# Kernel tuning notes

Measured on AMD Instinct MI355X. Metric: run time of the kernel, lower is better.

Reference implementation:

```python
import jax, jax.numpy as jnp
import numpy as np

HIDDEN = 512
NUM_HEADS = 8


def setup_inputs() -> dict:
    key = jax.random.key(0)
    ks = jax.random.split(key, 8)
    Tq, Tk, Cq, Ck, H = 1, 65536, 512, 512, HIDDEN
    s = 1.0 / np.sqrt(H)
    return {
        "Q": jax.random.normal(ks[0], (Tq, Cq), jnp.float32),
        "K": jax.random.normal(ks[1], (Tk, Ck), jnp.float32),
        "Wq": jax.random.normal(ks[2], (H, Cq), jnp.float32) * s,
        "bq": jax.random.normal(ks[3], (H,), jnp.float32) * s,
        "Wk": jax.random.normal(ks[4], (H, Ck), jnp.float32) * s,
        "bk": jax.random.normal(ks[5], (H,), jnp.float32) * s,
        "Wout": jax.random.normal(ks[6], (1, NUM_HEADS), jnp.float32) * 0.3,
        "bout": jax.random.normal(ks[7], (1,), jnp.float32) * 0.3,
    }


def reference(Q, K, Wq, bq, Wk, bk, Wout, bout):
    h = NUM_HEADS
    H = Wq.shape[0]
    d = H // h  # per-head dim
    # linear + ReLU projections
    Ql = jax.nn.relu(Q @ Wq.T + bq)          # [1, H]
    Kl = jax.nn.relu(K @ Wk.T + bk)          # [Tk, H]
    # split into heads (T_q == 1 is required by linear_out)
    Qh = Ql.reshape(h, d)                    # [h, d]
    Kh = Kl.reshape(-1, h, d)                # [Tk, h, d]
    # per-head scores, scaled by sqrt(d_head); dropout rate 0 -> identity
    scores = jnp.einsum('hd,thd->th', Qh, Kh) / (d ** 0.5)  # [Tk, h]
    # learned per-head fusion, then softmax over the T_k axis
    logits = scores @ Wout.T + bout          # [Tk, 1]
    return jax.nn.softmax(logits, axis=0)    # [Tk, 1]
```

## Files before the change

kernel.cpp:

```cpp
#include <hip/hip_runtime.h>
#include <hip/hip_fp16.h>

#define CDIM 512
#define ROWS 65536
#define BM   256

typedef _Float16 half8  __attribute__((ext_vector_type(8)));
typedef __fp16   fp16x2 __attribute__((ext_vector_type(2)));
typedef float    f32x16 __attribute__((ext_vector_type(16)));

#define GLD_LDS16(gp, lp) __builtin_amdgcn_global_load_lds( \
    (const __attribute__((address_space(1))) unsigned int*)(gp), \
    (__attribute__((address_space(3))) unsigned int*)(lp), 16, 0, 0)

__device__ __forceinline__ half8 cvt8(float4 f0, float4 f1) {
    union { fp16x2 h2[4]; half8 h8; } u;
    u.h2[0] = __builtin_amdgcn_cvt_pkrtz(f0.x, f0.y);
    u.h2[1] = __builtin_amdgcn_cvt_pkrtz(f0.z, f0.w);
    u.h2[2] = __builtin_amdgcn_cvt_pkrtz(f1.x, f1.y);
    u.h2[3] = __builtin_amdgcn_cvt_pkrtz(f1.z, f1.w);
    return u.h8;
}

__global__ void prep_kernel(const float* __restrict__ Q, const float* __restrict__ Wq,
                            const float* __restrict__ bq, const float* __restrict__ Wout,
                            const float* __restrict__ Wk,
                            float* __restrict__ v, _Float16* __restrict__ Wkf) {
    __shared__ float qs[CDIM];
    const int t = threadIdx.x;
    if (blockIdx.x < 32) {
        qs[t] = Q[t]; qs[t + 256] = Q[t + 256];
        __syncthreads();
        const int jj  = t >> 4;
        const int sub = t & 15;
        const int j   = blockIdx.x * 16 + jj;
        const float4* w4 = (const float4*)(Wq + (size_t)j * CDIM + sub * 32);
        const float4* q4 = (const float4*)(qs + sub * 32);
        float s = 0.f;
        #pragma unroll
        for (int i = 0; i < 8; ++i) {
            float4 w = w4[i]; float4 q = q4[i];
            s = fmaf(w.x, q.x, s); s = fmaf(w.y, q.y, s);
            s = fmaf(w.z, q.z, s); s = fmaf(w.w, q.w, s);
        }
        s += __shfl_xor(s, 1); s += __shfl_xor(s, 2);
        s += __shfl_xor(s, 4); s += __shfl_xor(s, 8);
        if (sub == 0) {
            s += bq[j];
            s = fmaxf(s, 0.f);
            v[j] = s * Wout[j >> 6] * 0.125f;
        }
    } else {
        const int gid = (blockIdx.x - 32) * 256 + t;
        const int jb  = gid >> 11;
        const int kc  = (gid >> 6) & 31;
        const int l   = gid & 63;
        const int j   = jb * 32 + (l & 31);
        const int k   = kc * 16 + (l >> 5) * 8;
        const float* src = Wk + (size_t)j * CDIM + k;
        float4 f0 = *(const float4*)(src);
        float4 f1 = *(const float4*)(src + 4);
        *(half8*)(Wkf + (size_t)gid * 8) = cvt8(f0, f1);
    }
}

__global__ __launch_bounds__(512, 1) void score_kernel(
    const float* __restrict__ Kmat, const _Float16* __restrict__ Wkf,
    const float* __restrict__ bk, const float* __restrict__ v,
    float* __restrict__ partial2)
{
    __shared__ alignas(16) char Ab[2][32768];
    __shared__ alignas(16) char Bbuf[2][32768];
    __shared__ float scr[2][4][128];

    const int tid  = threadIdx.x;
    const int lane = tid & 63;
    const int wave = tid >> 6;
    const int l31  = lane & 31;
    const int lhi  = lane >> 5;
    const int wm   = wave >> 2;
    const int wn   = wave & 3;
    const int cls  = blockIdx.y;
    const int rowbase = blockIdx.x * BM;

    const float* gA = Kmat + (size_t)(rowbase + wave * 32 + l31) * CDIM + lhi * 8;
    const _Float16* gB = Wkf + ((size_t)(cls * 8 + wave) * 32) * 512;

    f32x16 acc[4][2];
    #pragma unroll
    for (int mb = 0; mb < 4; ++mb)
        #pragma unroll
        for (int b = 0; b < 2; ++b)
            #pragma unroll
            for (int r = 0; r < 16; ++r) acc[mb][b][r] = 0.f;

    #pragma unroll
    for (int kc = 0; kc < 4; ++kc) {
        float4 f0 = *(const float4*)(gA + kc * 16);
        float4 f1 = *(const float4*)(gA + kc * 16 + 4);
        *(half8*)(Ab[0] + (wave * 4 + kc) * 1024 + lane * 16) = cvt8(f0, f1);
        GLD_LDS16(gB + (size_t)kc * 512 + lane * 8, Bbuf[0] + (wave * 4 + kc) * 1024);
    }
    float4 R[4][2];
    #pragma unroll
    for (int kc = 0; kc < 4; ++kc) {
        R[kc][0] = *(const float4*)(gA + 64 + kc * 16);
        R[kc][1] = *(const float4*)(gA + 64 + kc * 16 + 4);
    }
    __syncthreads();

    #pragma unroll
    for (int ks = 0; ks < 8; ++ks) {
        const int cur = ks & 1;
        if (ks < 7) {
            #pragma unroll
            for (int kc = 0; kc < 4; ++kc) {
                *(half8*)(Ab[cur ^ 1] + (wave * 4 + kc) * 1024 + lane * 16)
                    = cvt8(R[kc][0], R[kc][1]);
                GLD_LDS16(gB + (size_t)((ks + 1) * 4 + kc) * 512 + lane * 8,
                          Bbuf[cur ^ 1] + (wave * 4 + kc) * 1024);
            }
        }
        if (ks < 6) {
            #pragma unroll
            for (int kc = 0; kc < 4; ++kc) {
                R[kc][0] = *(const float4*)(gA + (ks + 2) * 64 + kc * 16);
                R[kc][1] = *(const float4*)(gA + (ks + 2) * 64 + kc * 16 + 4);
            }
        }
        __builtin_amdgcn_sched_barrier(0);
        #pragma unroll
        for (int kc = 0; kc < 4; ++kc) {
            half8 a0 = *(const half8*)(Ab[cur] + ((wm * 4 + 0) * 4 + kc) * 1024 + lane * 16);
            half8 a1 = *(const half8*)(Ab[cur] + ((wm * 4 + 1) * 4 + kc) * 1024 + lane * 16);
            half8 a2 = *(const half8*)(Ab[cur] + ((wm * 4 + 2) * 4 + kc) * 1024 + lane * 16);
            half8 a3 = *(const half8*)(Ab[cur] + ((wm * 4 + 3) * 4 + kc) * 1024 + lane * 16);
            half8 b0 = *(const half8*)(Bbuf[cur] + ((wn * 2 + 0) * 4 + kc) * 1024 + lane * 16);
            half8 b1 = *(const half8*)(Bbuf[cur] + ((wn * 2 + 1) * 4 + kc) * 1024 + lane * 16);
            acc[0][0] = __builtin_amdgcn_mfma_f32_32x32x16_f16(a0, b0, acc[0][0], 0, 0, 0);
            acc[1][0] = __builtin_amdgcn_mfma_f32_32x32x16_f16(a1, b0, acc[1][0], 0, 0, 0);
            acc[2][0] = __builtin_amdgcn_mfma_f32_32x32x16_f16(a2, b0, acc[2][0], 0, 0, 0);
            acc[3][0] = __builtin_amdgcn_mfma_f32_32x32x16_f16(a3, b0, acc[3][0], 0, 0, 0);
            acc[0][1] = __builtin_amdgcn_mfma_f32_32x32x16_f16(a0, b1, acc[0][1], 0, 0, 0);
            acc[1][1] = __builtin_amdgcn_mfma_f32_32x32x16_f16(a1, b1, acc[1][1], 0, 0, 0);
            acc[2][1] = __builtin_amdgcn_mfma_f32_32x32x16_f16(a2, b1, acc[2][1], 0, 0, 0);
            acc[3][1] = __builtin_amdgcn_mfma_f32_32x32x16_f16(a3, b1, acc[3][1], 0, 0, 0);
        }
        __syncthreads();
    }

    const int j0 = (cls * 8 + wn * 2 + 0) * 32 + l31;
    const int j1 = (cls * 8 + wn * 2 + 1) * 32 + l31;
    const float bj0 = bk[j0], vj0 = v[j0];
    const float bj1 = bk[j1], vj1 = v[j1];

    #pragma unroll
    for (int mb = 0; mb < 4; ++mb) {
        float part[16];
        #pragma unroll
        for (int r = 0; r < 16; ++r)
            part[r] = fmaxf(acc[mb][0][r] + bj0, 0.f) * vj0
                    + fmaxf(acc[mb][1][r] + bj1, 0.f) * vj1;

        float q0[8];
        #pragma unroll
        for (int i = 0; i < 8; ++i) {
            const bool b = lane & 1;
            float keep = b ? part[i + 8] : part[i];
            float send = b ? part[i] : part[i + 8];
            q0[i] = keep + __shfl_xor(send, 1);
        }
        float q1[4];
        #pragma unroll
        for (int i = 0; i < 4; ++i) {
            const bool b = lane & 2;
            float keep = b ? q0[i + 4] : q0[i];
            float send = b ? q0[i] : q0[i + 4];
            q1[i] = keep + __shfl_xor(send, 2);
        }
        float q2[2];
        #pragma unroll
        for (int i = 0; i < 2; ++i) {
            const bool b = lane & 4;
            float keep = b ? q1[i + 2] : q1[i];
            float send = b ? q1[i] : q1[i + 2];
            q2[i] = keep + __shfl_xor(send, 4);
        }
        float q3;
        {
            const bool b = lane & 8;
            float keep = b ? q2[1] : q2[0];
            float send = b ? q2[0] : q2[1];
            q3 = keep + __shfl_xor(send, 8);
        }
        float s = q3 + __shfl_xor(q3, 16);
        if (l31 < 16) {
            const int rr  = ((l31 & 1) << 3) | ((l31 & 2) << 1) | ((l31 & 4) >> 1) | ((l31 & 8) >> 3);
            const int row = (rr & 3) + 8 * (rr >> 2) + 4 * lhi;
            scr[wm][wn][mb * 32 + row] = s;
        }
    }
    __syncthreads();

    if (tid < 256) {
        const int wmx = tid >> 7;
        const int idx = tid & 127;
        float s = scr[wmx][0][idx] + scr[wmx][1][idx] + scr[wmx][2][idx] + scr[wmx][3][idx];
        partial2[(size_t)cls * ROWS + rowbase + wmx * 128 + idx] = s;
    }
}

__global__ void expsum_kernel(const float* __restrict__ partial2, float* __restrict__ logits,
                              float* __restrict__ blocksum) {
    __shared__ float red[256];
    const int t = threadIdx.x;
    const int row = blockIdx.x * 256 + t;
    const float lg = partial2[row] + partial2[ROWS + row];
    logits[row] = lg;
    red[t] = expf(lg);
    __syncthreads();
    for (int s = 128; s > 0; s >>= 1) {
        if (t < s) red[t] += red[t + s];
        __syncthreads();
    }
    if (t == 0) blocksum[blockIdx.x] = red[0];
}

__global__ void norm_kernel(const float* __restrict__ logits, const float* __restrict__ blocksum,
                            float* __restrict__ out) {
    __shared__ float red[256];
    const int t = threadIdx.x;
    red[t] = blocksum[t];
    __syncthreads();
    for (int s = 128; s > 0; s >>= 1) {
        if (t < s) red[t] += red[t + s];
        __syncthreads();
    }
    const float zinv = 1.0f / red[0];
    const int i = blockIdx.x * 256 + t;
    out[i] = expf(logits[i]) * zinv;
}

extern "C" void kernel_launch(void* const* d_in, const int* in_sizes, int n_in,
                              void* d_out, int out_size, void* d_ws, size_t ws_size,
                              hipStream_t stream) {
    const float* Q    = (const float*)d_in[0];
    const float* Kmat = (const float*)d_in[1];
    const float* Wq   = (const float*)d_in[2];
    const float* bq   = (const float*)d_in[3];
    const float* Wk   = (const float*)d_in[4];
    const float* bk   = (const float*)d_in[5];
    const float* Wout = (const float*)d_in[6];
    float* out = (float*)d_out;

    char* ws = (char*)d_ws;
    _Float16* Wkf   = (_Float16*)(ws);
    float* v        = (float*)(ws + 524288);
    float* partial2 = (float*)(ws + 526336);
    float* logits   = (float*)(ws + 1050624);
    float* blocksum = (float*)(ws + 1312768);

    hipLaunchKernelGGL(prep_kernel,   dim3(160),     dim3(256), 0, stream, Q, Wq, bq, Wout, Wk, v, Wkf);
    hipLaunchKernelGGL(score_kernel,  dim3(256, 2),  dim3(512), 0, stream, Kmat, Wkf, bk, v, partial2);
    hipLaunchKernelGGL(expsum_kernel, dim3(256),     dim3(256), 0, stream, partial2, logits, blocksum);
    hipLaunchKernelGGL(norm_kernel,   dim3(256),     dim3(256), 0, stream, logits, blocksum, out);
}
```

Before: 71.58 us.

## Shrink score GEMM tile to 128x256 with 256-thread blocks, two per CU

Restructures the score GEMM to use 128-row by 256-column tiles, 4 waves per block and 2 blocks per CU, with a 32-wide K step over 16 iterations instead of 64-wide over 8. Each wave now computes 2x4 MFMA tiles instead of 4x2. The A-tile fp16 conversion moves to after the MFMA loop, so global loads overlap compute. This is meant to double the grid to 1024 blocks and raise occupancy and latency hiding. In exchange there are more barriers, a shorter K depth per step, and the Wk tile is reloaded by twice as many blocks.

Result: faster. 64.57 us (-9.8%).

```diff
diff --git a/kernel.cpp b/kernel.cpp
--- a/kernel.cpp
+++ b/kernel.cpp
@@ -3,7 +3,7 @@
 
 #define CDIM 512
 #define ROWS 65536
-#define BM   256
+#define NSTEPS 16
 
 typedef _Float16 half8  __attribute__((ext_vector_type(8)));
 typedef __fp16   fp16x2 __attribute__((ext_vector_type(2)));
@@ -64,103 +64,119 @@
     }
 }
 
-__global__ __launch_bounds__(512, 1) void score_kernel(
+__global__ __launch_bounds__(256, 2) void score_kernel(
     const float* __restrict__ Kmat, const _Float16* __restrict__ Wkf,
     const float* __restrict__ bk, const float* __restrict__ v,
     float* __restrict__ partial2)
 {
-    __shared__ alignas(16) char Ab[2][32768];
-    __shared__ alignas(16) char Bbuf[2][32768];
-    __shared__ float scr[2][4][128];
+    __shared__ alignas(16) char Ab[2][8192];
+    __shared__ alignas(16) char Bb[2][16384];
+    __shared__ float scr[4][2][32];
 
     const int tid  = threadIdx.x;
     const int lane = tid & 63;
     const int wave = tid >> 6;
     const int l31  = lane & 31;
     const int lhi  = lane >> 5;
-    const int wm   = wave >> 2;
-    const int wn   = wave & 3;
+    const int wm   = wave >> 1;
+    const int wn   = wave & 1;
     const int cls  = blockIdx.y;
-    const int rowbase = blockIdx.x * BM;
+    const int rowbase = blockIdx.x * 128;
 
     const float* gA = Kmat + (size_t)(rowbase + wave * 32 + l31) * CDIM + lhi * 8;
-    const _Float16* gB = Wkf + ((size_t)(cls * 8 + wave) * 32) * 512;
-
-    f32x16 acc[4][2];
-    #pragma unroll
-    for (int mb = 0; mb < 4; ++mb)
-        #pragma unroll
-        for (int b = 0; b < 2; ++b)
-            #pragma unroll
-            for (int r = 0; r < 16; ++r) acc[mb][b][r] = 0.f;
-
-    #pragma unroll
-    for (int kc = 0; kc < 4; ++kc) {
-        float4 f0 = *(const float4*)(gA + kc * 16);
-        float4 f1 = *(const float4*)(gA + kc * 16 + 4);
-        *(half8*)(Ab[0] + (wave * 4 + kc) * 1024 + lane * 16) = cvt8(f0, f1);
-        GLD_LDS16(gB + (size_t)kc * 512 + lane * 8, Bbuf[0] + (wave * 4 + kc) * 1024);
-    }
-    float4 R[4][2];
-    #pragma unroll
-    for (int kc = 0; kc < 4; ++kc) {
-        R[kc][0] = *(const float4*)(gA + 64 + kc * 16);
-        R[kc][1] = *(const float4*)(gA + 64 + kc * 16 + 4);
-    }
-    __syncthreads();
-
-    #pragma unroll
-    for (int ks = 0; ks < 8; ++ks) {
+    const char* gB = (const char*)Wkf + (size_t)(cls * 8) * 32768;
+
+    f32x16 acc[2][4];
+    #pragma unroll
+    for (int mb = 0; mb < 2; ++mb)
+        #pragma unroll
+        for (int nb = 0; nb < 4; ++nb)
+            #pragma unroll
+            for (int r = 0; r < 16; ++r) acc[mb][nb][r] = 0.f;
+
+    #pragma unroll
+    for (int kcl = 0; kcl < 2; ++kcl) {
+        float4 f0 = *(const float4*)(gA + kcl * 16);
+        float4 f1 = *(const float4*)(gA + kcl * 16 + 4);
+        *(half8*)(Ab[0] + (wave * 2 + kcl) * 1024 + lane * 16) = cvt8(f0, f1);
+        #pragma unroll
+        for (int nbl = 0; nbl < 2; ++nbl) {
+            const int nb = wave * 2 + nbl;
+            GLD_LDS16(gB + ((size_t)nb * 32 + kcl) * 1024 + lane * 16,
+                      Bb[0] + (nb * 2 + kcl) * 1024 + lane * 16);
+        }
+    }
+    __syncthreads();
+
+    float4 R[2][2];
+
+    for (int ks = 0; ks < NSTEPS; ++ks) {
         const int cur = ks & 1;
-        if (ks < 7) {
-            #pragma unroll
-            for (int kc = 0; kc < 4; ++kc) {
-                *(half8*)(Ab[cur ^ 1] + (wave * 4 + kc) * 1024 + lane * 16)
-                    = cvt8(R[kc][0], R[kc][1]);
-                GLD_LDS16(gB + (size_t)((ks + 1) * 4 + kc) * 512 + lane * 8,
-                          Bbuf[cur ^ 1] + (wave * 4 + kc) * 1024);
+        const bool pf = (ks + 1 < NSTEPS);
+
+        if (pf) {
+            const float* ga = gA + (ks + 1) * 32;
+            #pragma unroll
+            for (int kcl = 0; kcl < 2; ++kcl) {
+                R[kcl][0] = *(const float4*)(ga + kcl * 16);
+                R[kcl][1] = *(const float4*)(ga + kcl * 16 + 4);
+                #pragma unroll
+                for (int nbl = 0; nbl < 2; ++nbl) {
+                    const int nb = wave * 2 + nbl;
+                    GLD_LDS16(gB + ((size_t)nb * 32 + (ks + 1) * 2 + kcl) * 1024 + lane * 16,
+                              Bb[cur ^ 1] + (nb * 2 + kcl) * 1024 + lane * 16);
+                }
             }
         }
-        if (ks < 6) {
-            #pragma unroll
-            for (int kc = 0; kc < 4; ++kc) {
-                R[kc][0] = *(const float4*)(gA + (ks + 2) * 64 + kc * 16);
-                R[kc][1] = *(const float4*)(gA + (ks + 2) * 64 + kc * 16 + 4);
-            }
-        }
         __builtin_amdgcn_sched_barrier(0);
-        #pragma unroll
-        for (int kc = 0; kc < 4; ++kc) {
-            half8 a0 = *(const half8*)(Ab[cur] + ((wm * 4 + 0) * 4 + kc) * 1024 + lane * 16);
-            half8 a1 = *(const half8*)(Ab[cur] + ((wm * 4 + 1) * 4 + kc) * 1024 + lane * 16);
-            half8 a2 = *(const half8*)(Ab[cur] + ((wm * 4 + 2) * 4 + kc) * 1024 + lane * 16);
-            half8 a3 = *(const half8*)(Ab[cur] + ((wm * 4 + 3) * 4 + kc) * 1024 + lane * 16);
-            half8 b0 = *(const half8*)(Bbuf[cur] + ((wn * 2 + 0) * 4 + kc) * 1024 + lane * 16);
-            half8 b1 = *(const half8*)(Bbuf[cur] + ((wn * 2 + 1) * 4 + kc) * 1024 + lane * 16);
+
+        #pragma unroll
+        for (int kcl = 0; kcl < 2; ++kcl) {
+            half8 a0 = *(const half8*)(Ab[cur] + ((wm * 2 + 0) * 2 + kcl) * 1024 + lane * 16);
+            half8 a1 = *(const half8*)(Ab[cur] + ((wm * 2 + 1) * 2 + kcl) * 1024 + lane * 16);
+            half8 b0 = *(const half8*)(Bb[cur] + ((wn * 4 + 0) * 2 + kcl) * 1024 + lane * 16);
+            half8 b1 = *(const half8*)(Bb[cur] + ((wn * 4 + 1) * 2 + kcl) * 1024 + lane * 16);
+            half8 b2 = *(const half8*)(Bb[cur] + ((wn * 4 + 2) * 2 + kcl) * 1024 + lane * 16);
+            half8 b3 = *(const half8*)(Bb[cur] + ((wn * 4 + 3) * 2 + kcl) * 1024 + lane * 16);
             acc[0][0] = __builtin_amdgcn_mfma_f32_32x32x16_f16(a0, b0, acc[0][0], 0, 0, 0);
+            acc[0][1] = __builtin_amdgcn_mfma_f32_32x32x16_f16(a0, b1, acc[0][1], 0, 0, 0);
+            acc[0][2] = __builtin_amdgcn_mfma_f32_32x32x16_f16(a0, b2, acc[0][2], 0, 0, 0);
+            acc[0][3] = __builtin_amdgcn_mfma_f32_32x32x16_f16(a0, b3, acc[0][3], 0, 0, 0);
             acc[1][0] = __builtin_amdgcn_mfma_f32_32x32x16_f16(a1, b0, acc[1][0], 0, 0, 0);
-            acc[2][0] = __builtin_amdgcn_mfma_f32_32x32x16_f16(a2, b0, acc[2][0], 0, 0, 0);
-            acc[3][0] = __builtin_amdgcn_mfma_f32_32x32x16_f16(a3, b0, acc[3][0], 0, 0, 0);
-            acc[0][1] = __builtin_amdgcn_mfma_f32_32x32x16_f16(a0, b1, acc[0][1], 0, 0, 0);
             acc[1][1] = __builtin_amdgcn_mfma_f32_32x32x16_f16(a1, b1, acc[1][1], 0, 0, 0);
-            acc[2][1] = __builtin_amdgcn_mfma_f32_32x32x16_f16(a2, b1, acc[2][1], 0, 0, 0);
-            acc[3][1] = __builtin_amdgcn_mfma_f32_32x32x16_f16(a3, b1, acc[3][1], 0, 0, 0);
-        }
-        __syncthreads();
-    }
-
-    const int j0 = (cls * 8 + wn * 2 + 0) * 32 + l31;
-    const int j1 = (cls * 8 + wn * 2 + 1) * 32 + l31;
-    const float bj0 = bk[j0], vj0 = v[j0];
-    const float bj1 = bk[j1], vj1 = v[j1];
-
-    #pragma unroll
-    for (int mb = 0; mb < 4; ++mb) {
+            acc[1][2] = __builtin_amdgcn_mfma_f32_32x32x16_f16(a1, b2, acc[1][2], 0, 0, 0);
+            acc[1][3] = __builtin_amdgcn_mfma_f32_32x32x16_f16(a1, b3, acc[1][3], 0, 0, 0);
+        }
+        __builtin_amdgcn_sched_barrier(0);
+
+        if (pf) {
+            #pragma unroll
+            for (int kcl = 0; kcl < 2; ++kcl)
+                *(half8*)(Ab[cur ^ 1] + (wave * 2 + kcl) * 1024 + lane * 16)
+                    = cvt8(R[kcl][0], R[kcl][1]);
+        }
+        __syncthreads();
+    }
+
+    float bj[4], vj[4];
+    #pragma unroll
+    for (int nb = 0; nb < 4; ++nb) {
+        const int j = cls * 256 + (wn * 4 + nb) * 32 + l31;
+        bj[nb] = bk[j];
+        vj[nb] = v[j];
+    }
+
+    #pragma unroll
+    for (int mb = 0; mb < 2; ++mb) {
         float part[16];
         #pragma unroll
-        for (int r = 0; r < 16; ++r)
-            part[r] = fmaxf(acc[mb][0][r] + bj0, 0.f) * vj0
-                    + fmaxf(acc[mb][1][r] + bj1, 0.f) * vj1;
+        for (int r = 0; r < 16; ++r) {
+            float s = 0.f;
+            #pragma unroll
+            for (int nb = 0; nb < 4; ++nb)
+                s += fmaxf(acc[mb][nb][r] + bj[nb], 0.f) * vj[nb];
+            part[r] = s;
+        }
 
         float q0[8];
         #pragma unroll
@@ -197,16 +213,15 @@
         if (l31 < 16) {
             const int rr  = ((l31 & 1) << 3) | ((l31 & 2) << 1) | ((l31 & 4) >> 1) | ((l31 & 8) >> 3);
             const int row = (rr & 3) + 8 * (rr >> 2) + 4 * lhi;
-            scr[wm][wn][mb * 32 + row] = s;
-        }
-    }
-    __syncthreads();
-
-    if (tid < 256) {
-        const int wmx = tid >> 7;
-        const int idx = tid & 127;
-        float s = scr[wmx][0][idx] + scr[wmx][1][idx] + scr[wmx][2][idx] + scr[wmx][3][idx];
-        partial2[(size_t)cls * ROWS + rowbase + wmx * 128 + idx] = s;
+            scr[wm * 2 + mb][wn][row] = s;
+        }
+    }
+    __syncthreads();
+
+    if (tid < 128) {
+        const int rb = tid >> 5;
+        const int r  = tid & 31;
+        partial2[(size_t)cls * ROWS + rowbase + rb * 32 + r] = scr[rb][0][r] + scr[rb][1][r];
     }
 }
 
@@ -261,7 +276,7 @@
     float* blocksum = (float*)(ws + 1312768);
 
     hipLaunchKernelGGL(prep_kernel,   dim3(160),     dim3(256), 0, stream, Q, Wq, bq, Wout, Wk, v, Wkf);
-    hipLaunchKernelGGL(score_kernel,  dim3(256, 2),  dim3(512), 0, stream, Kmat, Wkf, bk, v, partial2);
+    hipLaunchKernelGGL(score_kernel,  dim3(512, 2),  dim3(256), 0, stream, Kmat, Wkf, bk, v, partial2);
     hipLaunchKernelGGL(expsum_kernel, dim3(256),     dim3(256), 0, stream, partial2, logits, blocksum);
     hipLaunchKernelGGL(norm_kernel,   dim3(256),     dim3(256), 0, stream, logits, blocksum, out);
 }
```
